# Kernel optimization log

Measured on AMD Instinct MI355X. Metric: run time of the kernel, lower is better.

Reference implementation:

```python
import jax, jax.numpy as jnp
import numpy as np

TOP_K = 4  # config.ffn_config.moe_top_k


def setup_inputs() -> dict:
    key = jax.random.key(0)
    k1, k2, k3, k4 = jax.random.split(key, 4)
    T, D, I, E = 4096, 1024, 2048, 16
    hidden_states = jax.random.normal(k1, (T, D), dtype=jnp.float32)
    router_w = jax.random.normal(k2, (E, D), dtype=jnp.float32) * 0.02
    # ws stacks [w1; v1] along output dim: [E, 2*I, D]
    ws = jax.random.normal(k3, (E, 2 * I, D), dtype=jnp.float32) * 0.02
    # w2s: [E, D, I]
    w2s = jax.random.normal(k4, (E, D, I), dtype=jnp.float32) * 0.02
    return {"hidden_states": hidden_states, "router_w": router_w, "ws": ws, "w2s": w2s}


def reference(hidden_states, router_w, ws, w2s):
    T, D = hidden_states.shape
    E = router_w.shape[0]
    I = ws.shape[1] // 2

    # Router: ReplicatedLinear(d_model -> num_experts), no bias
    router_logits = hidden_states @ router_w.T                      # [T, E]

    # fused_moe gating: softmax over all experts, top-k, renormalize
    probs = jax.nn.softmax(router_logits, axis=-1)                  # [T, E]
    topk_vals, topk_idx = jax.lax.top_k(probs, TOP_K)               # [T, K]
    topk_vals = topk_vals / jnp.sum(topk_vals, axis=-1, keepdims=True)
    # dense gate matrix [T, E]: selected experts get renormalized weight, else 0
    gates = jnp.zeros((T, E), dtype=hidden_states.dtype)
    gates = gates.at[jnp.arange(T)[:, None], topk_idx].set(topk_vals)

    h = jnp.einsum('td,eid->tei', hidden_states, ws)                # [T, E, 2I]
    act = jax.nn.silu(h[..., :I]) * h[..., I:]                      # [T, E, I]
    y = jnp.einsum('tei,edi->ted', act, w2s)                        # [T, E, D]

    # Combine: weighted sum over selected experts
    return jnp.einsum('ted,te->td', y, gates)                       # [T, D]
```

## Files before the change

kernel.cpp:

```cpp
#include <hip/hip_runtime.h>
#include <hip/hip_bf16.h>

#define T_TOK 4096
#define D_MODEL 1024
#define I_DIM 2048
#define E_EXP 16

typedef __bf16 bf16x8 __attribute__((ext_vector_type(8)));
typedef float f32x4 __attribute__((ext_vector_type(4)));

__device__ __forceinline__ bf16x8 pack8(f32x4 a, f32x4 b) {
    bf16x8 r;
    r[0] = (__bf16)a[0]; r[1] = (__bf16)a[1]; r[2] = (__bf16)a[2]; r[3] = (__bf16)a[3];
    r[4] = (__bf16)b[0]; r[5] = (__bf16)b[1]; r[6] = (__bf16)b[2]; r[7] = (__bf16)b[3];
    return r;
}

__device__ __forceinline__ void gl2lds(const __bf16* src, __bf16* dst) {
    __builtin_amdgcn_global_load_lds(
        (const __attribute__((address_space(1))) unsigned int*)src,
        (__attribute__((address_space(3))) unsigned int*)dst, 16, 0, 0);
}

__global__ __launch_bounds__(256) void cvt_kernel(
    const float* __restrict__ in, __bf16* __restrict__ out, int n8)
{
    const int stride = gridDim.x * 256;
    for (int i = blockIdx.x * 256 + threadIdx.x; i < n8; i += stride) {
        f32x4 a = ((const f32x4*)in)[i * 2];
        f32x4 b = ((const f32x4*)in)[i * 2 + 1];
        ((bf16x8*)out)[i] = pack8(a, b);
    }
}

__global__ __launch_bounds__(256) void router_fused_kernel(
    const float* __restrict__ x, const float* __restrict__ rw,
    unsigned int* __restrict__ choices, float* __restrict__ gate4,
    __bf16* __restrict__ x_bf, const float* __restrict__ wsw, __bf16* __restrict__ ws_bf)
{
    const int b = blockIdx.x;
    if (b >= 1280) {
        const int n8 = E_EXP * 2 * I_DIM * D_MODEL / 8;
        for (int i = (b - 1280) * 256 + threadIdx.x; i < n8; i += 2048 * 256) {
            f32x4 a = ((const f32x4*)wsw)[i * 2];
            f32x4 c = ((const f32x4*)wsw)[i * 2 + 1];
            ((bf16x8*)ws_bf)[i] = pack8(a, c);
        }
        return;
    }
    if (b >= 1024) {
        const int n8 = T_TOK * D_MODEL / 8;
        for (int i = (b - 1024) * 256 + threadIdx.x; i < n8; i += 256 * 256) {
            f32x4 a = ((const f32x4*)x)[i * 2];
            f32x4 c = ((const f32x4*)x)[i * 2 + 1];
            ((bf16x8*)x_bf)[i] = pack8(a, c);
        }
        return;
    }
    const int wid = threadIdx.x >> 6, lane = threadIdx.x & 63;
    const int t = b * 4 + wid;
    const int e = lane & 15, part = lane >> 4;

    const float* xr = x + (size_t)t * D_MODEL + part * 256;
    const float* wr = rw + (size_t)e * D_MODEL + part * 256;
    double acc = 0.0;
    #pragma unroll 4
    for (int i = 0; i < 256; i += 4) {
        f32x4 xv = *(const f32x4*)(xr + i);
        f32x4 wv = *(const f32x4*)(wr + i);
        acc += (double)xv[0] * wv[0] + (double)xv[1] * wv[1]
             + (double)xv[2] * wv[2] + (double)xv[3] * wv[3];
    }
    acc += __shfl_xor(acc, 16, 64);
    acc += __shfl_xor(acc, 32, 64);

    __shared__ float logits[4][16];
    if (lane < 16) logits[wid][lane] = (float)acc;
    __syncthreads();

    if (lane == 0) {
        float l[16];
        #pragma unroll
        for (int i = 0; i < 16; i++) l[i] = logits[wid][i];
        int idx[4]; float val[4];
        unsigned taken = 0;
        for (int k = 0; k < 4; k++) {
            int best = 0; float bv = -1e30f;
            for (int i = 0; i < 16; i++)
                if (!((taken >> i) & 1) && l[i] > bv) { bv = l[i]; best = i; }
            idx[k] = best; val[k] = bv; taken |= (1u << best);
        }
        const float m = val[0];
        float w[4], s = 0.f;
        for (int k = 0; k < 4; k++) { w[k] = __expf(val[k] - m); s += w[k]; }
        choices[t] = (unsigned)idx[0] | ((unsigned)idx[1] << 4)
                   | ((unsigned)idx[2] << 8) | ((unsigned)idx[3] << 12);
        f32x4 g = {w[0] / s, w[1] / s, w[2] / s, w[3] / s};
        *(f32x4*)(gate4 + t * 4) = g;
    }
}

__global__ __launch_bounds__(256) void build_lists_kernel(
    const unsigned int* __restrict__ choices, const float* __restrict__ gate4,
    int* __restrict__ counts, int* __restrict__ tok_list, float* __restrict__ gate_list,
    int* __restrict__ kidx_list)
{
    const int e = blockIdx.x;
    const int tid = threadIdx.x, lane = tid & 63, w = tid >> 6;
    __shared__ int wave_cnt[4];
    __shared__ int running;
    if (tid == 0) running = 0;
    __syncthreads();
    for (int chunk = 0; chunk < T_TOK; chunk += 256) {
        const int t = chunk + tid;
        const unsigned int ch = choices[t];
        int k = -1;
        #pragma unroll
        for (int kk = 0; kk < 4; ++kk)
            if (((ch >> (4 * kk)) & 15u) == (unsigned)e) k = kk;
        const unsigned long long m = __ballot(k >= 0);
        const int my = __popcll(m & ((1ull << lane) - 1ull));
        if (lane == 0) wave_cnt[w] = __popcll(m);
        __syncthreads();
        int base = running;
        #pragma unroll
        for (int i = 0; i < 4; ++i) if (i < w) base += wave_cnt[i];
        if (k >= 0) {
            const int slot = base + my;
            tok_list[e * T_TOK + slot] = t;
            gate_list[e * T_TOK + slot] = gate4[t * 4 + k];
            kidx_list[e * T_TOK + slot] = k;
        }
        __syncthreads();
        if (tid == 0) running += wave_cnt[0] + wave_cnt[1] + wave_cnt[2] + wave_cnt[3];
        __syncthreads();
    }
    if (tid == 0) counts[e] = running;
}

__global__ void prefix_kernel(const int* __restrict__ counts, int* __restrict__ prefix) {
    if (threadIdx.x == 0) {
        int acc = 0;
        for (int e = 0; e < E_EXP; e++) { prefix[e] = acc; acc += (counts[e] + 255) & ~255; }
        prefix[E_EXP] = acc;
    }
}

__global__ __launch_bounds__(256, 3) void gemm1_kernel(
    const __bf16* __restrict__ xb, const __bf16* __restrict__ wsb,
    const int* __restrict__ counts, const int* __restrict__ prefix,
    const int* __restrict__ tok_list, __bf16* __restrict__ act)
{
    const int q8 = gridDim.x >> 3;
    const int lid = (blockIdx.x & 7) * q8 + (blockIdx.x >> 3);
    const int e = lid >> 9;
    const int r = lid & 511;
    const int tileM = r & 15;
    const int tileN = r >> 4;

    const int count = counts[e];
    if (tileM * 128 >= count) return;

    const int tid = threadIdx.x;
    const int lane = tid & 63, w = tid >> 6;
    const int l15 = lane & 15, q = lane >> 4, l7 = lane & 7;
    const int wm = w >> 1, wc = w & 1;

    __shared__ __bf16 As[128 * 64];
    __shared__ __bf16 Bs[128 * 64];

    const int rl = lane >> 3;
    const int lc = (lane & 7) ^ rl;
    const __bf16* ptrA[4]; const __bf16* ptrB[4];
    #pragma unroll
    for (int i = 0; i < 4; ++i) {
        int grow = tileM * 128 + w * 32 + i * 8 + rl;
        if (grow >= count) grow = count - 1;
        const int token = tok_list[e * T_TOK + grow];
        ptrA[i] = xb + (size_t)token * D_MODEL + lc * 8;
        const int sub = w * 32 + i * 8 + rl;
        const int gcol = (sub < 64) ? (tileN * 64 + sub) : (I_DIM + tileN * 64 + (sub - 64));
        ptrB[i] = wsb + ((size_t)e * 2 * I_DIM + gcol) * D_MODEL + lc * 8;
    }
    __bf16* dA = &As[w * 2048];
    __bf16* dB = &Bs[w * 2048];

    #define STAGE(koff) do { \
        _Pragma("unroll") \
        for (int i_ = 0; i_ < 4; ++i_) gl2lds(ptrA[i_] + (koff), dA + i_ * 512); \
        _Pragma("unroll") \
        for (int i_ = 0; i_ < 4; ++i_) gl2lds(ptrB[i_] + (koff), dB + i_ * 512); \
    } while (0)

    f32x4 acc[4][4];
    const f32x4 z = {0.f, 0.f, 0.f, 0.f};
    #pragma unroll
    for (int mi = 0; mi < 4; ++mi)
        #pragma unroll
        for (int nj = 0; nj < 4; ++nj) acc[mi][nj] = z;

    const int c0 = (q ^ l7) * 8, c1 = ((4 + q) ^ l7) * 8;
    const int aoff = (wm * 64 + l15) * 64;
    const int boff = (wc * 32 + l15) * 64;

    STAGE(0);
    for (int kt = 0; kt < 16; ++kt) {
        __syncthreads();
        bf16x8 a0[4], a1[4], b0[4], b1[4];
        #pragma unroll
        for (int mi = 0; mi < 4; ++mi) {
            a0[mi] = *(const bf16x8*)&As[aoff + mi * 1024 + c0];
            a1[mi] = *(const bf16x8*)&As[aoff + mi * 1024 + c1];
        }
        #pragma unroll
        for (int nj = 0; nj < 2; ++nj) {
            b0[nj]     = *(const bf16x8*)&Bs[boff + nj * 1024 + c0];
            b0[nj + 2] = *(const bf16x8*)&Bs[boff + 4096 + nj * 1024 + c0];
            b1[nj]     = *(const bf16x8*)&Bs[boff + nj * 1024 + c1];
            b1[nj + 2] = *(const bf16x8*)&Bs[boff + 4096 + nj * 1024 + c1];
        }
        __syncthreads();
        if (kt + 1 < 16) STAGE((kt + 1) * 64);
        #pragma unroll
        for (int mi = 0; mi < 4; ++mi)
            #pragma unroll
            for (int nj = 0; nj < 4; ++nj) {
                acc[mi][nj] = __builtin_amdgcn_mfma_f32_16x16x32_bf16(a0[mi], b0[nj], acc[mi][nj], 0, 0, 0);
                acc[mi][nj] = __builtin_amdgcn_mfma_f32_16x16x32_bf16(a1[mi], b1[nj], acc[mi][nj], 0, 0, 0);
            }
    }
    #undef STAGE

    const int abase = prefix[e];
    #pragma unroll
    for (int mi = 0; mi < 4; ++mi) {
        #pragma unroll
        for (int j = 0; j < 4; ++j) {
            const int grow = tileM * 128 + wm * 64 + mi * 16 + q * 4 + j;
            if (grow < count) {
                __bf16* arowp = act + (size_t)(abase + grow) * I_DIM + tileN * 64 + wc * 32 + l15;
                #pragma unroll
                for (int nj = 0; nj < 2; ++nj) {
                    const float v1 = acc[mi][nj][j];
                    const float v2 = acc[mi][nj + 2][j];
                    arowp[nj * 16] = (__bf16)(v1 / (1.f + __expf(-v1)) * v2);
                }
            }
        }
    }
}

__global__ __launch_bounds__(256, 3) void gemm2_kernel(
    const __bf16* __restrict__ act, const __bf16* __restrict__ w2b,
    const int* __restrict__ counts, const int* __restrict__ prefix,
    const int* __restrict__ tok_list, const float* __restrict__ gate_list,
    const int* __restrict__ kidx_list, float* __restrict__ ypart)
{
    const int q8 = gridDim.x >> 3;
    const int lid = (blockIdx.x & 7) * q8 + (blockIdx.x >> 3);
    const int e = lid >> 7;
    const int r = lid & 127;
    const int tileM = r & 15;
    const int tileN = r >> 4;

    const int count = counts[e];
    if (tileM * 128 >= count) return;

    const int tid = threadIdx.x;
    const int lane = tid & 63, w = tid >> 6;
    const int l15 = lane & 15, q = lane >> 4, l7 = lane & 7;
    const int wm = w >> 1, wc = w & 1;
    const int abase = prefix[e];

    __shared__ __bf16 As[128 * 64];
    __shared__ __bf16 Bs[128 * 64];

    const int rl = lane >> 3;
    const int lc = (lane & 7) ^ rl;
    const __bf16* ptrA[4]; const __bf16* ptrB[4];
    #pragma unroll
    for (int i = 0; i < 4; ++i) {
        const int ar = tileM * 128 + w * 32 + i * 8 + rl;
        ptrA[i] = act + (size_t)(abase + ar) * I_DIM + lc * 8;
        const int dcol = tileN * 128 + w * 32 + i * 8 + rl;
        ptrB[i] = w2b + ((size_t)e * D_MODEL + dcol) * I_DIM + lc * 8;
    }
    __bf16* dA = &As[w * 2048];
    __bf16* dB = &Bs[w * 2048];

    #define STAGE(koff) do { \
        _Pragma("unroll") \
        for (int i_ = 0; i_ < 4; ++i_) gl2lds(ptrA[i_] + (koff), dA + i_ * 512); \
        _Pragma("unroll") \
        for (int i_ = 0; i_ < 4; ++i_) gl2lds(ptrB[i_] + (koff), dB + i_ * 512); \
    } while (0)

    f32x4 acc[4][4];
    const f32x4 z = {0.f, 0.f, 0.f, 0.f};
    #pragma unroll
    for (int mi = 0; mi < 4; ++mi)
        #pragma unroll
        for (int nj = 0; nj < 4; ++nj) acc[mi][nj] = z;

    const int c0 = (q ^ l7) * 8, c1 = ((4 + q) ^ l7) * 8;
    const int aoff = (wm * 64 + l15) * 64;
    const int boff = (wc * 64 + l15) * 64;

    STAGE(0);
    for (int kt = 0; kt < 32; ++kt) {
        __syncthreads();
        bf16x8 a0[4], a1[4], b0[4], b1[4];
        #pragma unroll
        for (int mi = 0; mi < 4; ++mi) {
            a0[mi] = *(const bf16x8*)&As[aoff + mi * 1024 + c0];
            a1[mi] = *(const bf16x8*)&As[aoff + mi * 1024 + c1];
        }
        #pragma unroll
        for (int nj = 0; nj < 4; ++nj) {
            b0[nj] = *(const bf16x8*)&Bs[boff + nj * 1024 + c0];
            b1[nj] = *(const bf16x8*)&Bs[boff + nj * 1024 + c1];
        }
        __syncthreads();
        if (kt + 1 < 32) STAGE((kt + 1) * 64);
        #pragma unroll
        for (int mi = 0; mi < 4; ++mi)
            #pragma unroll
            for (int nj = 0; nj < 4; ++nj) {
                acc[mi][nj] = __builtin_amdgcn_mfma_f32_16x16x32_bf16(a0[mi], b0[nj], acc[mi][nj], 0, 0, 0);
                acc[mi][nj] = __builtin_amdgcn_mfma_f32_16x16x32_bf16(a1[mi], b1[nj], acc[mi][nj], 0, 0, 0);
            }
    }
    #undef STAGE

    #pragma unroll
    for (int mi = 0; mi < 4; ++mi) {
        #pragma unroll
        for (int j = 0; j < 4; ++j) {
            const int grow = tileM * 128 + wm * 64 + mi * 16 + q * 4 + j;
            if (grow < count) {
                const int token = tok_list[e * T_TOK + grow];
                const int kk = kidx_list[e * T_TOK + grow];
                const float gate = gate_list[e * T_TOK + grow];
                float* orow = ypart + ((size_t)token * 4 + kk) * D_MODEL + tileN * 128 + wc * 64 + l15;
                #pragma unroll
                for (int nj = 0; nj < 4; ++nj)
                    orow[nj * 16] = gate * acc[mi][nj][j];
            }
        }
    }
}

__global__ __launch_bounds__(256) void combine_kernel(
    const float* __restrict__ ypart, float* __restrict__ out)
{
    const int t = blockIdx.x;
    const int d = threadIdx.x * 4;
    const float* p = ypart + (size_t)t * 4 * D_MODEL;
    f32x4 s = *(const f32x4*)(p + d);
    s += *(const f32x4*)(p + D_MODEL + d);
    s += *(const f32x4*)(p + 2 * D_MODEL + d);
    s += *(const f32x4*)(p + 3 * D_MODEL + d);
    *(f32x4*)(out + (size_t)t * D_MODEL + d) = s;
}

extern "C" void kernel_launch(void* const* d_in, const int* in_sizes, int n_in,
                              void* d_out, int out_size, void* d_ws, size_t ws_size,
                              hipStream_t stream)
{
    const float* x   = (const float*)d_in[0];
    const float* rw  = (const float*)d_in[1];
    const float* wsw = (const float*)d_in[2];
    const float* w2s = (const float*)d_in[3];
    float* out = (float*)d_out;

    char* wsb = (char*)d_ws;
    int* counts        = (int*)wsb;
    int* prefix        = (int*)(wsb + 128);
    int* tok_list      = (int*)(wsb + 1024);
    float* gate_list   = (float*)(wsb + 1024 + E_EXP * T_TOK * 4);
    unsigned* choices  = (unsigned*)(wsb + 544u * 1024);
    float* gate4       = (float*)(wsb + 576u * 1024);
    int* kidx_list     = (int*)(wsb + 640u * 1024);
    __bf16* x_bf       = (__bf16*)(wsb + (1u << 20));
    __bf16* act        = (__bf16*)(wsb + (12u << 20));
    __bf16* ws_bf      = (__bf16*)(wsb + (96u << 20));
    __bf16* w2_bf      = ws_bf;
    float* ypart       = (float*)(wsb + (160u << 20));

    router_fused_kernel<<<dim3(3328), 256, 0, stream>>>(x, rw, choices, gate4, x_bf, wsw, ws_bf);
    build_lists_kernel<<<dim3(E_EXP), 256, 0, stream>>>(choices, gate4, counts, tok_list, gate_list, kidx_list);
    prefix_kernel<<<1, 64, 0, stream>>>(counts, prefix);

    gemm1_kernel<<<dim3(8192), 256, 0, stream>>>(
        x_bf, ws_bf, counts, prefix, tok_list, act);

    cvt_kernel<<<8192, 256, 0, stream>>>(w2s, w2_bf, E_EXP * D_MODEL * I_DIM / 8);

    gemm2_kernel<<<dim3(2048), 256, 0, stream>>>(
        act, w2_bf, counts, prefix, tok_list, gate_list, kidx_list, ypart);

    combine_kernel<<<dim3(T_TOK), 256, 0, stream>>>(ypart, out);
}
```

Baseline: 444.0 us.

## Fuse w2 fp32-to-bf16 conversion into gemm2 B-tile loading with register prefetch

```diff
diff --git a/kernel.cpp b/kernel.cpp
--- a/kernel.cpp
+++ b/kernel.cpp
@@ -20,17 +20,6 @@
     __builtin_amdgcn_global_load_lds(
         (const __attribute__((address_space(1))) unsigned int*)src,
         (__attribute__((address_space(3))) unsigned int*)dst, 16, 0, 0);
-}
-
-__global__ __launch_bounds__(256) void cvt_kernel(
-    const float* __restrict__ in, __bf16* __restrict__ out, int n8)
-{
-    const int stride = gridDim.x * 256;
-    for (int i = blockIdx.x * 256 + threadIdx.x; i < n8; i += stride) {
-        f32x4 a = ((const f32x4*)in)[i * 2];
-        f32x4 b = ((const f32x4*)in)[i * 2 + 1];
-        ((bf16x8*)out)[i] = pack8(a, b);
-    }
 }
 
 __global__ __launch_bounds__(256) void router_fused_kernel(
@@ -251,7 +240,7 @@
 }
 
 __global__ __launch_bounds__(256, 3) void gemm2_kernel(
-    const __bf16* __restrict__ act, const __bf16* __restrict__ w2b,
+    const __bf16* __restrict__ act, const float* __restrict__ w2f,
     const int* __restrict__ counts, const int* __restrict__ prefix,
     const int* __restrict__ tok_list, const float* __restrict__ gate_list,
     const int* __restrict__ kidx_list, float* __restrict__ ypart)
@@ -276,23 +265,37 @@
     __shared__ __bf16 Bs[128 * 64];
 
     const int rl = lane >> 3;
-    const int lc = (lane & 7) ^ rl;
-    const __bf16* ptrA[4]; const __bf16* ptrB[4];
+    const int j8 = lane & 7;
+    const int lc = j8 ^ rl;
+    const __bf16* ptrA[4];
+    const float* ptrBf[4];
     #pragma unroll
     for (int i = 0; i < 4; ++i) {
         const int ar = tileM * 128 + w * 32 + i * 8 + rl;
         ptrA[i] = act + (size_t)(abase + ar) * I_DIM + lc * 8;
         const int dcol = tileN * 128 + w * 32 + i * 8 + rl;
-        ptrB[i] = w2b + ((size_t)e * D_MODEL + dcol) * I_DIM + lc * 8;
+        ptrBf[i] = w2f + ((size_t)e * D_MODEL + dcol) * I_DIM + lc * 8;
     }
     __bf16* dA = &As[w * 2048];
-    __bf16* dB = &Bs[w * 2048];
-
-    #define STAGE(koff) do { \
+    const int bwr = w * 2048 + rl * 64 + j8 * 8;
+
+    f32x4 bIn[4][2];
+
+    #define STAGE_A(koff) do { \
         _Pragma("unroll") \
         for (int i_ = 0; i_ < 4; ++i_) gl2lds(ptrA[i_] + (koff), dA + i_ * 512); \
+    } while (0)
+    #define STAGE_B_LOAD(koff) do { \
         _Pragma("unroll") \
-        for (int i_ = 0; i_ < 4; ++i_) gl2lds(ptrB[i_] + (koff), dB + i_ * 512); \
+        for (int i_ = 0; i_ < 4; ++i_) { \
+            bIn[i_][0] = *(const f32x4*)(ptrBf[i_] + (koff)); \
+            bIn[i_][1] = *(const f32x4*)(ptrBf[i_] + (koff) + 4); \
+        } \
+    } while (0)
+    #define STAGE_B_WRITE() do { \
+        _Pragma("unroll") \
+        for (int i_ = 0; i_ < 4; ++i_) \
+            *(bf16x8*)&Bs[bwr + i_ * 512] = pack8(bIn[i_][0], bIn[i_][1]); \
     } while (0)
 
     f32x4 acc[4][4];
@@ -306,7 +309,11 @@
     const int aoff = (wm * 64 + l15) * 64;
     const int boff = (wc * 64 + l15) * 64;
 
-    STAGE(0);
+    STAGE_B_LOAD(0);
+    STAGE_B_WRITE();
+    STAGE_B_LOAD(64);
+    STAGE_A(0);
+
     for (int kt = 0; kt < 32; ++kt) {
         __syncthreads();
         bf16x8 a0[4], a1[4], b0[4], b1[4];
@@ -321,7 +328,11 @@
             b1[nj] = *(const bf16x8*)&Bs[boff + nj * 1024 + c1];
         }
         __syncthreads();
-        if (kt + 1 < 32) STAGE((kt + 1) * 64);
+        if (kt + 1 < 32) {
+            STAGE_B_WRITE();
+            if (kt + 2 < 32) STAGE_B_LOAD((kt + 2) * 64);
+            STAGE_A((kt + 1) * 64);
+        }
         #pragma unroll
         for (int mi = 0; mi < 4; ++mi)
             #pragma unroll
@@ -330,7 +341,9 @@
                 acc[mi][nj] = __builtin_amdgcn_mfma_f32_16x16x32_bf16(a1[mi], b1[nj], acc[mi][nj], 0, 0, 0);
             }
     }
-    #undef STAGE
+    #undef STAGE_A
+    #undef STAGE_B_LOAD
+    #undef STAGE_B_WRITE
 
     #pragma unroll
     for (int mi = 0; mi < 4; ++mi) {
@@ -384,7 +397,6 @@
     __bf16* x_bf       = (__bf16*)(wsb + (1u << 20));
     __bf16* act        = (__bf16*)(wsb + (12u << 20));
     __bf16* ws_bf      = (__bf16*)(wsb + (96u << 20));
-    __bf16* w2_bf      = ws_bf;
     float* ypart       = (float*)(wsb + (160u << 20));
 
     router_fused_kernel<<<dim3(3328), 256, 0, stream>>>(x, rw, choices, gate4, x_bf, wsw, ws_bf);
@@ -394,10 +406,8 @@
     gemm1_kernel<<<dim3(8192), 256, 0, stream>>>(
         x_bf, ws_bf, counts, prefix, tok_list, act);
 
-    cvt_kernel<<<8192, 256, 0, stream>>>(w2s, w2_bf, E_EXP * D_MODEL * I_DIM / 8);
-
     gemm2_kernel<<<dim3(2048), 256, 0, stream>>>(
-        act, w2_bf, counts, prefix, tok_list, gate_list, kidx_list, ypart);
+        act, w2s, counts, prefix, tok_list, gate_list, kidx_list, ypart);
 
     combine_kernel<<<dim3(T_TOK), 256, 0, stream>>>(ypart, out);
 }
```

After: 476.1 us. 1.07x slower.

## Restructure gemm1 into 256x256 tiles with double-buffered LDS ping-pong pipeline

Applied to the files above, without the earlier changes.

```diff
diff --git a/kernel.cpp b/kernel.cpp
--- a/kernel.cpp
+++ b/kernel.cpp
@@ -20,6 +20,10 @@
     __builtin_amdgcn_global_load_lds(
         (const __attribute__((address_space(1))) unsigned int*)src,
         (__attribute__((address_space(3))) unsigned int*)dst, 16, 0, 0);
+}
+
+__device__ __forceinline__ f32x4 mf(bf16x8 a, bf16x8 b, f32x4 c) {
+    return __builtin_amdgcn_mfma_f32_16x16x32_bf16(a, b, c, 0, 0, 0);
 }
 
 __global__ __launch_bounds__(256) void cvt_kernel(
@@ -146,104 +150,239 @@
     }
 }
 
-__global__ __launch_bounds__(256, 3) void gemm1_kernel(
+__global__ __launch_bounds__(512) void gemm1_kernel(
     const __bf16* __restrict__ xb, const __bf16* __restrict__ wsb,
     const int* __restrict__ counts, const int* __restrict__ prefix,
     const int* __restrict__ tok_list, __bf16* __restrict__ act)
 {
     const int q8 = gridDim.x >> 3;
     const int lid = (blockIdx.x & 7) * q8 + (blockIdx.x >> 3);
-    const int e = lid >> 9;
-    const int r = lid & 511;
-    const int tileM = r & 15;
-    const int tileN = r >> 4;
+    const int e = lid >> 7;
+    const int r = lid & 127;
+    const int tileM = r & 7;
+    const int tileN = r >> 3;
 
     const int count = counts[e];
-    if (tileM * 128 >= count) return;
+    if (tileM * 256 >= count) return;
 
     const int tid = threadIdx.x;
     const int lane = tid & 63, w = tid >> 6;
     const int l15 = lane & 15, q = lane >> 4, l7 = lane & 7;
-    const int wm = w >> 1, wc = w & 1;
-
-    __shared__ __bf16 As[128 * 64];
-    __shared__ __bf16 Bs[128 * 64];
+    const int wm = w >> 2, wn = w & 3;
+
+    __shared__ __bf16 As[2][256 * 64];
+    __shared__ __bf16 Bs[2][256 * 64];
 
     const int rl = lane >> 3;
     const int lc = (lane & 7) ^ rl;
-    const __bf16* ptrA[4]; const __bf16* ptrB[4];
+    const __bf16* pA[2][2]; const __bf16* pB[2][2];
     #pragma unroll
-    for (int i = 0; i < 4; ++i) {
-        int grow = tileM * 128 + w * 32 + i * 8 + rl;
-        if (grow >= count) grow = count - 1;
-        const int token = tok_list[e * T_TOK + grow];
-        ptrA[i] = xb + (size_t)token * D_MODEL + lc * 8;
-        const int sub = w * 32 + i * 8 + rl;
-        const int gcol = (sub < 64) ? (tileN * 64 + sub) : (I_DIM + tileN * 64 + (sub - 64));
-        ptrB[i] = wsb + ((size_t)e * 2 * I_DIM + gcol) * D_MODEL + lc * 8;
-    }
-    __bf16* dA = &As[w * 2048];
-    __bf16* dB = &Bs[w * 2048];
-
-    #define STAGE(koff) do { \
-        _Pragma("unroll") \
-        for (int i_ = 0; i_ < 4; ++i_) gl2lds(ptrA[i_] + (koff), dA + i_ * 512); \
-        _Pragma("unroll") \
-        for (int i_ = 0; i_ < 4; ++i_) gl2lds(ptrB[i_] + (koff), dB + i_ * 512); \
-    } while (0)
-
-    f32x4 acc[4][4];
+    for (int h = 0; h < 2; ++h) {
+        #pragma unroll
+        for (int i = 0; i < 2; ++i) {
+            int grow = tileM * 256 + h * 128 + w * 16 + i * 8 + rl;
+            if (grow >= count) grow = count - 1;
+            const int token = tok_list[e * T_TOK + grow];
+            pA[h][i] = xb + (size_t)token * D_MODEL + lc * 8;
+            const int rr = h * 128 + w * 16 + i * 8 + rl;
+            const int f = rr >> 4;
+            const int cidx = (f >> 1) * 16 + (rr & 15);
+            const int gcol = (f & 1) ? (I_DIM + tileN * 128 + cidx)
+                                     : (tileN * 128 + cidx);
+            pB[h][i] = wsb + ((size_t)e * 2 * I_DIM + gcol) * D_MODEL + lc * 8;
+        }
+    }
+
+    #define STGA(bf, h, ko) do { \
+        gl2lds(pA[h][0] + (ko), &As[bf][((h) * 128 + w * 16) * 64]); \
+        gl2lds(pA[h][1] + (ko), &As[bf][((h) * 128 + w * 16) * 64 + 512]); } while (0)
+    #define STGB(bf, h, ko) do { \
+        gl2lds(pB[h][0] + (ko), &Bs[bf][((h) * 128 + w * 16) * 64]); \
+        gl2lds(pB[h][1] + (ko), &Bs[bf][((h) * 128 + w * 16) * 64 + 512]); } while (0)
+    #define BAR()   asm volatile("s_barrier" ::: "memory")
+    #define LGKM0() do { asm volatile("s_waitcnt lgkmcnt(0)" ::: "memory"); \
+                         __builtin_amdgcn_sched_barrier(0); } while (0)
+    #define VM(n)   asm volatile("s_waitcnt vmcnt(" #n ")" ::: "memory")
+
+    f32x4 acc[8][4];
     const f32x4 z = {0.f, 0.f, 0.f, 0.f};
     #pragma unroll
-    for (int mi = 0; mi < 4; ++mi)
+    for (int mi = 0; mi < 8; ++mi)
         #pragma unroll
         for (int nj = 0; nj < 4; ++nj) acc[mi][nj] = z;
 
     const int c0 = (q ^ l7) * 8, c1 = ((4 + q) ^ l7) * 8;
-    const int aoff = (wm * 64 + l15) * 64;
-    const int boff = (wc * 32 + l15) * 64;
-
-    STAGE(0);
-    for (int kt = 0; kt < 16; ++kt) {
-        __syncthreads();
-        bf16x8 a0[4], a1[4], b0[4], b1[4];
+    const int ar0 = (wm * 128 + l15) * 64;
+    const int br0 = (wn * 64 + l15) * 64;
+
+    STGA(0, 0, 0); STGA(0, 1, 0); STGB(0, 0, 0); STGB(0, 1, 0);
+    STGB(1, 0, 64); STGA(1, 0, 64);
+    VM(4); BAR();
+
+    bf16x8 aF[4][2], bE[2][2], bO[2][2];
+
+    for (int it = 0; it < 8; ++it) {
+        const int T = it * 2;
+        const bool st2 = (it < 7);
         #pragma unroll
         for (int mi = 0; mi < 4; ++mi) {
-            a0[mi] = *(const bf16x8*)&As[aoff + mi * 1024 + c0];
-            a1[mi] = *(const bf16x8*)&As[aoff + mi * 1024 + c1];
+            aF[mi][0] = *(const bf16x8*)&As[0][ar0 + mi * 1024 + c0];
+            aF[mi][1] = *(const bf16x8*)&As[0][ar0 + mi * 1024 + c1];
         }
         #pragma unroll
         for (int nj = 0; nj < 2; ++nj) {
-            b0[nj]     = *(const bf16x8*)&Bs[boff + nj * 1024 + c0];
-            b0[nj + 2] = *(const bf16x8*)&Bs[boff + 4096 + nj * 1024 + c0];
-            b1[nj]     = *(const bf16x8*)&Bs[boff + nj * 1024 + c1];
-            b1[nj + 2] = *(const bf16x8*)&Bs[boff + 4096 + nj * 1024 + c1];
-        }
-        __syncthreads();
-        if (kt + 1 < 16) STAGE((kt + 1) * 64);
-        #pragma unroll
-        for (int mi = 0; mi < 4; ++mi)
-            #pragma unroll
-            for (int nj = 0; nj < 4; ++nj) {
-                acc[mi][nj] = __builtin_amdgcn_mfma_f32_16x16x32_bf16(a0[mi], b0[nj], acc[mi][nj], 0, 0, 0);
-                acc[mi][nj] = __builtin_amdgcn_mfma_f32_16x16x32_bf16(a1[mi], b1[nj], acc[mi][nj], 0, 0, 0);
-            }
-    }
-    #undef STAGE
+            bE[nj][0] = *(const bf16x8*)&Bs[0][br0 + nj * 1024 + c0];
+            bE[nj][1] = *(const bf16x8*)&Bs[0][br0 + nj * 1024 + c1];
+        }
+        STGA(1, 1, (T + 1) * 64);
+        BAR(); LGKM0();
+        __builtin_amdgcn_s_setprio(1);
+        #pragma unroll
+        for (int mi = 0; mi < 4; ++mi)
+            #pragma unroll
+            for (int nj = 0; nj < 2; ++nj) {
+                acc[mi][nj] = mf(aF[mi][0], bE[nj][0], acc[mi][nj]);
+                acc[mi][nj] = mf(aF[mi][1], bE[nj][1], acc[mi][nj]);
+            }
+        __builtin_amdgcn_s_setprio(0);
+        BAR();
+        #pragma unroll
+        for (int nj = 0; nj < 2; ++nj) {
+            bO[nj][0] = *(const bf16x8*)&Bs[0][br0 + (2 + nj) * 1024 + c0];
+            bO[nj][1] = *(const bf16x8*)&Bs[0][br0 + (2 + nj) * 1024 + c1];
+        }
+        STGB(1, 1, (T + 1) * 64);
+        BAR(); LGKM0();
+        __builtin_amdgcn_s_setprio(1);
+        #pragma unroll
+        for (int mi = 0; mi < 4; ++mi)
+            #pragma unroll
+            for (int nj = 0; nj < 2; ++nj) {
+                acc[mi][2 + nj] = mf(aF[mi][0], bO[nj][0], acc[mi][2 + nj]);
+                acc[mi][2 + nj] = mf(aF[mi][1], bO[nj][1], acc[mi][2 + nj]);
+            }
+        __builtin_amdgcn_s_setprio(0);
+        BAR();
+        #pragma unroll
+        for (int mi = 0; mi < 4; ++mi) {
+            aF[mi][0] = *(const bf16x8*)&As[0][ar0 + (4 + mi) * 1024 + c0];
+            aF[mi][1] = *(const bf16x8*)&As[0][ar0 + (4 + mi) * 1024 + c1];
+        }
+        if (st2) STGB(0, 0, (T + 2) * 64);
+        BAR(); LGKM0();
+        __builtin_amdgcn_s_setprio(1);
+        #pragma unroll
+        for (int mi = 0; mi < 4; ++mi)
+            #pragma unroll
+            for (int nj = 0; nj < 2; ++nj) {
+                acc[4 + mi][nj] = mf(aF[mi][0], bE[nj][0], acc[4 + mi][nj]);
+                acc[4 + mi][nj] = mf(aF[mi][1], bE[nj][1], acc[4 + mi][nj]);
+            }
+        __builtin_amdgcn_s_setprio(0);
+        BAR();
+        if (st2) STGA(0, 0, (T + 2) * 64);
+        BAR(); LGKM0();
+        __builtin_amdgcn_s_setprio(1);
+        #pragma unroll
+        for (int mi = 0; mi < 4; ++mi)
+            #pragma unroll
+            for (int nj = 0; nj < 2; ++nj) {
+                acc[4 + mi][2 + nj] = mf(aF[mi][0], bO[nj][0], acc[4 + mi][2 + nj]);
+                acc[4 + mi][2 + nj] = mf(aF[mi][1], bO[nj][1], acc[4 + mi][2 + nj]);
+            }
+        __builtin_amdgcn_s_setprio(0);
+        if (it == 7) { VM(0); } else { VM(4); }
+        BAR();
+        #pragma unroll
+        for (int mi = 0; mi < 4; ++mi) {
+            aF[mi][0] = *(const bf16x8*)&As[1][ar0 + mi * 1024 + c0];
+            aF[mi][1] = *(const bf16x8*)&As[1][ar0 + mi * 1024 + c1];
+        }
+        #pragma unroll
+        for (int nj = 0; nj < 2; ++nj) {
+            bE[nj][0] = *(const bf16x8*)&Bs[1][br0 + nj * 1024 + c0];
+            bE[nj][1] = *(const bf16x8*)&Bs[1][br0 + nj * 1024 + c1];
+        }
+        if (st2) STGA(0, 1, (T + 2) * 64);
+        BAR(); LGKM0();
+        __builtin_amdgcn_s_setprio(1);
+        #pragma unroll
+        for (int mi = 0; mi < 4; ++mi)
+            #pragma unroll
+            for (int nj = 0; nj < 2; ++nj) {
+                acc[mi][nj] = mf(aF[mi][0], bE[nj][0], acc[mi][nj]);
+                acc[mi][nj] = mf(aF[mi][1], bE[nj][1], acc[mi][nj]);
+            }
+        __builtin_amdgcn_s_setprio(0);
+        BAR();
+        #pragma unroll
+        for (int nj = 0; nj < 2; ++nj) {
+            bO[nj][0] = *(const bf16x8*)&Bs[1][br0 + (2 + nj) * 1024 + c0];
+            bO[nj][1] = *(const bf16x8*)&Bs[1][br0 + (2 + nj) * 1024 + c1];
+        }
+        if (st2) STGB(0, 1, (T + 2) * 64);
+        BAR(); LGKM0();
+        __builtin_amdgcn_s_setprio(1);
+        #pragma unroll
+        for (int mi = 0; mi < 4; ++mi)
+            #pragma unroll
+            for (int nj = 0; nj < 2; ++nj) {
+                acc[mi][2 + nj] = mf(aF[mi][0], bO[nj][0], acc[mi][2 + nj]);
+                acc[mi][2 + nj] = mf(aF[mi][1], bO[nj][1], acc[mi][2 + nj]);
+            }
+        __builtin_amdgcn_s_setprio(0);
+        BAR();
+        #pragma unroll
+        for (int mi = 0; mi < 4; ++mi) {
+            aF[mi][0] = *(const bf16x8*)&As[1][ar0 + (4 + mi) * 1024 + c0];
+            aF[mi][1] = *(const bf16x8*)&As[1][ar0 + (4 + mi) * 1024 + c1];
+        }
+        if (st2) STGB(1, 0, (T + 3) * 64);
+        BAR(); LGKM0();
+        __builtin_amdgcn_s_setprio(1);
+        #pragma unroll
+        for (int mi = 0; mi < 4; ++mi)
+            #pragma unroll
+            for (int nj = 0; nj < 2; ++nj) {
+                acc[4 + mi][nj] = mf(aF[mi][0], bE[nj][0], acc[4 + mi][nj]);
+                acc[4 + mi][nj] = mf(aF[mi][1], bE[nj][1], acc[4 + mi][nj]);
+            }
+        __builtin_amdgcn_s_setprio(0);
+        BAR();
+        if (st2) STGA(1, 0, (T + 3) * 64);
+        BAR(); LGKM0();
+        __builtin_amdgcn_s_setprio(1);
+        #pragma unroll
+        for (int mi = 0; mi < 4; ++mi)
+            #pragma unroll
+            for (int nj = 0; nj < 2; ++nj) {
+                acc[4 + mi][2 + nj] = mf(aF[mi][0], bO[nj][0], acc[4 + mi][2 + nj]);
+                acc[4 + mi][2 + nj] = mf(aF[mi][1], bO[nj][1], acc[4 + mi][2 + nj]);
+            }
+        __builtin_amdgcn_s_setprio(0);
+        if (it == 7) { VM(0); } else { VM(4); }
+        BAR();
+    }
+    #undef STGA
+    #undef STGB
+    #undef BAR
+    #undef LGKM0
+    #undef VM
 
     const int abase = prefix[e];
     #pragma unroll
-    for (int mi = 0; mi < 4; ++mi) {
+    for (int mi = 0; mi < 8; ++mi) {
         #pragma unroll
         for (int j = 0; j < 4; ++j) {
-            const int grow = tileM * 128 + wm * 64 + mi * 16 + q * 4 + j;
+            const int grow = tileM * 256 + wm * 128 + mi * 16 + q * 4 + j;
             if (grow < count) {
-                __bf16* arowp = act + (size_t)(abase + grow) * I_DIM + tileN * 64 + wc * 32 + l15;
+                __bf16* arowp = act + (size_t)(abase + grow) * I_DIM
+                              + tileN * 128 + wn * 32 + l15;
                 #pragma unroll
-                for (int nj = 0; nj < 2; ++nj) {
-                    const float v1 = acc[mi][nj][j];
-                    const float v2 = acc[mi][nj + 2][j];
-                    arowp[nj * 16] = (__bf16)(v1 / (1.f + __expf(-v1)) * v2);
+                for (int p = 0; p < 2; ++p) {
+                    const float v1 = acc[mi][2 * p][j];
+                    const float v2 = acc[mi][2 * p + 1][j];
+                    arowp[p * 16] = (__bf16)(v1 / (1.f + __expf(-v1)) * v2);
                 }
             }
         }
@@ -326,8 +465,8 @@
         for (int mi = 0; mi < 4; ++mi)
             #pragma unroll
             for (int nj = 0; nj < 4; ++nj) {
-                acc[mi][nj] = __builtin_amdgcn_mfma_f32_16x16x32_bf16(a0[mi], b0[nj], acc[mi][nj], 0, 0, 0);
-                acc[mi][nj] = __builtin_amdgcn_mfma_f32_16x16x32_bf16(a1[mi], b1[nj], acc[mi][nj], 0, 0, 0);
+                acc[mi][nj] = mf(a0[mi], b0[nj], acc[mi][nj]);
+                acc[mi][nj] = mf(a1[mi], b1[nj], acc[mi][nj]);
             }
     }
     #undef STAGE
@@ -391,7 +530,7 @@
     build_lists_kernel<<<dim3(E_EXP), 256, 0, stream>>>(choices, gate4, counts, tok_list, gate_list, kidx_list);
     prefix_kernel<<<1, 64, 0, stream>>>(counts, prefix);
 
-    gemm1_kernel<<<dim3(8192), 256, 0, stream>>>(
+    gemm1_kernel<<<dim3(2048), 512, 0, stream>>>(
         x_bf, ws_bf, counts, prefix, tok_list, act);
 
     cvt_kernel<<<8192, 256, 0, stream>>>(w2s, w2_bf, E_EXP * D_MODEL * I_DIM / 8);
```

After: 522.5 us. 17.7% more time.
